# Performance work log

Hardware: AMD Instinct MI355X
Metric: run time of the kernel (lower is better)

Reference implementation:

```python
import jax, jax.numpy as jnp
import numpy as np

NUM_HEADS = 4
LN_EPS = 1e-5
ALPHA_SCALE = 2.0


def setup_inputs() -> dict:
    key = jax.random.key(0)
    ks = jax.random.split(key, 8)
    bs, C, H, W = 64, 256, 56, 56
    T, D = 6, 192
    HW = H * W
    w = lambda k, shape: (jax.random.normal(k, shape, jnp.float32) * 0.02)
    return {
        "features": jax.random.normal(ks[0], (bs, C, H, W), jnp.float32),
        "tokens": jax.random.normal(ks[1], (T, bs, D), jnp.float32),
        # mlp: Linear(HW -> T)
        "mlp_w": w(ks[2], (T, HW)), "mlp_b": jnp.zeros((T,), jnp.float32),
        # q: Linear(D -> C)
        "q_w": w(ks[3], (C, D)), "q_b": jnp.zeros((C,), jnp.float32),
        # alpha: Linear(D -> C)
        "alpha_w": w(ks[4], (C, D)), "alpha_b": jnp.zeros((C,), jnp.float32),
        # proj: Linear(C -> D)
        "proj_w": w(ks[5], (D, C)), "proj_b": jnp.zeros((D,), jnp.float32),
        "ln_g": jnp.ones((D,), jnp.float32), "ln_b": jnp.zeros((D,), jnp.float32),
    }


def reference(features, tokens, mlp_w, mlp_b, q_w, q_b,
              alpha_w, alpha_b, proj_w, proj_b, ln_g, ln_b):
    bs, C, H, W = features.shape
    T, _, D = tokens.shape
    h = NUM_HEADS
    dh = C // h
    HW = H * W
    scale = dh ** -0.5

    f = features.reshape(bs, C, HW)

    # mlp branch: Linear over HW -> [bs, C, T] -> permute to [T, bs, C]
    t_sum = jnp.einsum('bcn,tn->tbc', f, mlp_w) + mlp_b[:, None, None]

    # attn branch: few tokens attend over H*W feature map (k reused as v)
    q = jnp.einsum('tbd,cd->tbc', tokens, q_w) + q_b          # [T, bs, C]
    q = q.reshape(T, bs, h, dh).transpose(1, 2, 0, 3)         # [bs, h, T, dh]
    k = f.reshape(bs, h, dh, HW)                              # [bs, h, dh, HW]
    attn = jnp.einsum('bhtd,bhdn->bhtn', q, k) * scale        # [bs, h, T, HW]
    a = jax.nn.softmax(attn, axis=-1)
    attn_out = jnp.einsum('bhtn,bhdn->bhtd', a, k)            # [bs, h, T, dh]
    t_a = attn_out.transpose(2, 0, 1, 3).reshape(T, bs, C)
    t_sum = t_sum + t_a

    # dynamic gate: h_sigmoid(alpha(tokens)) * 2.0
    alp = jnp.clip(jnp.einsum('tbd,cd->tbc', tokens, alpha_w) + alpha_b + 3.0,
                   0.0, 6.0) / 6.0 * ALPHA_SCALE              # [T, bs, C]
    t_sum = t_sum * alp

    # proj + residual + LayerNorm (post-norm, drop_path rate 0 -> identity)
    t_sum = jnp.einsum('tbc,dc->tbd', t_sum, proj_w) + proj_b  # [T, bs, D]
    tok = tokens + t_sum
    mu = tok.mean(-1, keepdims=True)
    var = ((tok - mu) ** 2).mean(-1, keepdims=True)
    tok = (tok - mu) * jax.lax.rsqrt(var + LN_EPS) * ln_g + ln_b

    return tok, attn.reshape(bs, h, T, H, W)
```

## Files before the change

### kernel.cpp

```cpp
#include <hip/hip_runtime.h>
#include <hip/hip_bf16.h>

constexpr int BS = 64, C = 256, NH = 4, DH = 64, T = 6, D = 192;
constexpr int HW = 3136;
constexpr int NT = 112;
constexpr int S = 4, CPB = 7;
constexpr int PNF = 136;
constexpr int PNS = 116;
constexpr int QP = 72;
constexpr float SCALE = 0.125f;
constexpr float LN_EPS = 1e-5f;

typedef short bf16x8 __attribute__((ext_vector_type(8)));
typedef float f32x4 __attribute__((ext_vector_type(4)));

__device__ inline unsigned short f2bf(float x) {
    union { float f; unsigned u; } v; v.f = x;
    unsigned r = v.u + 0x7FFFu + ((v.u >> 16) & 1u);
    return (unsigned short)(r >> 16);
}

__device__ inline void st_bf8(unsigned short* dst, float4 p) {
    unsigned lo = (unsigned)f2bf(p.x) | ((unsigned)f2bf(p.y) << 16);
    unsigned hi = (unsigned)f2bf(p.z) | ((unsigned)f2bf(p.w) << 16);
    *(uint2*)dst = make_uint2(lo, hi);
}

__device__ inline int fsw(int r, int n) { return n ^ (((r >> 3) & 3) << 4); }

__device__ inline void wg_barrier_lgkm() {
    asm volatile("s_waitcnt lgkmcnt(0)" ::: "memory");
    __builtin_amdgcn_s_barrier();
    asm volatile("" ::: "memory");
}

__global__ __launch_bounds__(256) void qalpha_kernel(
    const float* __restrict__ tokens,
    const float* __restrict__ q_w,
    const float* __restrict__ q_b,
    const float* __restrict__ alpha_w,
    const float* __restrict__ alpha_b,
    float* __restrict__ q_ws,
    float* __restrict__ alp_ws)
{
    int b = blockIdx.x;
    int c = threadIdx.x;
    __shared__ float tok_s[T][D];
    for (int i = c; i < T * (D / 4); i += 256) {
        int t = i / (D / 4), v = i % (D / 4);
        *(float4*)&tok_s[t][4 * v] =
            *(const float4*)&tokens[((size_t)t * BS + b) * D + 4 * v];
    }
    __syncthreads();

    const float4* qr = (const float4*)(q_w + (size_t)c * D);
    const float4* ar = (const float4*)(alpha_w + (size_t)c * D);
    float accq[T] = {0, 0, 0, 0, 0, 0};
    float acca[T] = {0, 0, 0, 0, 0, 0};
    for (int v = 0; v < D / 4; ++v) {
        float4 qw4 = qr[v], aw4 = ar[v];
#pragma unroll
        for (int t = 0; t < T; ++t) {
            float4 t4 = *(const float4*)&tok_s[t][4 * v];
            accq[t] += qw4.x * t4.x + qw4.y * t4.y + qw4.z * t4.z + qw4.w * t4.w;
            acca[t] += aw4.x * t4.x + aw4.y * t4.y + aw4.z * t4.z + aw4.w * t4.w;
        }
    }
    float qb = q_b[c], ab = alpha_b[c];
#pragma unroll
    for (int t = 0; t < T; ++t) {
        size_t idx = ((size_t)t * BS + b) * C + c;
        q_ws[idx] = accq[t] + qb;
        float aa = acca[t] + ab + 3.0f;
        alp_ws[idx] = fminf(fmaxf(aa, 0.0f), 6.0f) * (2.0f / 6.0f);
    }
}

struct PF { float4 f0, f1, f2, f3, f4, m; };

__global__ __launch_bounds__(384) void fused_attn_mlp(
    const float* __restrict__ feat,
    const float* __restrict__ mlp_w,
    const float* __restrict__ q_ws,
    float* __restrict__ out_attn,
    float* __restrict__ o_part,
    float* __restrict__ mlp_part,
    float* __restrict__ ml_part)
{
    int bh = blockIdx.x / S, sp = blockIdx.x % S;
    int b = bh / NH, h = bh % NH;
    int tid = threadIdx.x;
    int wave = tid >> 6, lane = tid & 63;
    int col = lane & 15, quad = lane >> 4;

    __shared__ unsigned short fch[DH][PNF];
    __shared__ unsigned short pw[16][PNF];
    __shared__ unsigned short qs[16][QP];
    __shared__ float st[T][PNS];
    __shared__ float m_s[T], l_s[T], al_s[T];

    const float* fbase = feat + ((size_t)b * C + h * DH) * HW;
    float* obase = out_attn + ((size_t)bh * T) * HW;

    const int o0 = (tid / 28) * HW + 4 * (tid % 28);
    const int o1 = ((tid + 384) / 28) * HW + 4 * ((tid + 384) % 28);
    const int o2 = ((tid + 768) / 28) * HW + 4 * ((tid + 768) % 28);
    const int o3 = ((tid + 1152) / 28) * HW + 4 * ((tid + 1152) % 28);
    const int o4 = ((tid + 1536) / 28) * HW + 4 * ((tid + 1536) % 28);

    auto pf_issue = [&](PF& p, int n0) {
        p.f0 = *(const float4*)&fbase[o0 + n0];
        p.f1 = *(const float4*)&fbase[o1 + n0];
        p.f2 = *(const float4*)&fbase[o2 + n0];
        p.f3 = *(const float4*)&fbase[o3 + n0];
        if (tid < 256) p.f4 = *(const float4*)&fbase[o4 + n0];
        if (tid < 168) p.m  = *(const float4*)&mlp_w[o0 + n0];
    };
    auto pf_commit = [&](const PF& p) {
        int r0 = tid / 28,          c0 = 4 * (tid % 28);
        int r1 = (tid + 384) / 28,  c1 = 4 * ((tid + 384) % 28);
        int r2 = (tid + 768) / 28,  c2 = 4 * ((tid + 768) % 28);
        int r3 = (tid + 1152) / 28, c3 = 4 * ((tid + 1152) % 28);
        st_bf8(&fch[r0][fsw(r0, c0)], p.f0);
        st_bf8(&fch[r1][fsw(r1, c1)], p.f1);
        st_bf8(&fch[r2][fsw(r2, c2)], p.f2);
        st_bf8(&fch[r3][fsw(r3, c3)], p.f3);
        if (tid < 256) {
            int r4 = (tid + 1536) / 28, c4 = 4 * ((tid + 1536) % 28);
            st_bf8(&fch[r4][fsw(r4, c4)], p.f4);
        }
        if (tid < 168) {
            int rm = 6 + tid / 28, cm = 4 * (tid % 28);
            st_bf8(&pw[rm][fsw(rm, cm)], p.m);
        }
    };

    const int nsp = sp * CPB * NT;
    PF A;
    pf_issue(A, nsp);

    for (int i = tid; i < 16 * PNF; i += 384) pw[i / PNF][i % PNF] = 0;
    for (int i = tid; i < DH * 16; i += 384) {
        int r = i / 16;
        fch[r][fsw(r, 112 + (i % 16))] = 0;
    }
    if (tid < T) { m_s[tid] = -3e38f; l_s[tid] = 0.f; }
    qs[wave][lane] = f2bf(q_ws[((size_t)wave * BS + b) * C + h * DH + lane]);

    f32x4 accPW = {0.f, 0.f, 0.f, 0.f};
    wg_barrier_lgkm();

#pragma unroll 1
    for (int cc = 0; cc < CPB; ++cc) {
        const int n0 = nsp + cc * NT;

        pf_commit(A);
        if (cc + 1 < CPB) pf_issue(A, n0 + NT);
        wg_barrier_lgkm();

        for (int tile = wave; tile < 7; tile += 6) {
            bf16x8 a0 = *(const bf16x8*)&qs[col][quad * 8];
            bf16x8 a1 = *(const bf16x8*)&qs[col][32 + quad * 8];
            int nsw = (tile * 16 + col) ^ (quad << 4);
            bf16x8 b0, b1;
#pragma unroll
            for (int j = 0; j < 8; ++j) {
                b0[j] = (short)fch[quad * 8 + j][nsw];
                b1[j] = (short)fch[32 + quad * 8 + j][nsw];
            }
            f32x4 acc = {0.f, 0.f, 0.f, 0.f};
            acc = __builtin_amdgcn_mfma_f32_16x16x32_bf16(a0, b0, acc, 0, 0, 0);
            acc = __builtin_amdgcn_mfma_f32_16x16x32_bf16(a1, b1, acc, 0, 0, 0);
#pragma unroll
            for (int reg = 0; reg < 4; ++reg) {
                int r = quad * 4 + reg;
                if (r < 6) st[r][tile * 16 + col] = acc[reg] * SCALE;
            }
        }
        wg_barrier_lgkm();

        {
            int t = wave;
            float v0 = st[t][lane];
            float v1 = (lane + 64 < NT) ? st[t][lane + 64] : -3e38f;
            float mloc = fmaxf(v0, v1);
#pragma unroll
            for (int off = 32; off; off >>= 1) mloc = fmaxf(mloc, __shfl_down(mloc, off));
            mloc = __shfl(mloc, 0);
            float m_old = m_s[t], m_new = fmaxf(m_old, mloc);
            float p0 = __expf(v0 - m_new);
            float p1 = (lane + 64 < NT) ? __expf(v1 - m_new) : 0.f;
            pw[t][lane] = f2bf(p0);
            if (lane + 64 < NT) pw[t][lane + 64] = f2bf(p1);
            float ssum = p0 + p1;
#pragma unroll
            for (int off = 32; off; off >>= 1) ssum += __shfl_down(ssum, off);
            if (lane == 0) {
                float alpha = __expf(m_old - m_new);
                l_s[t] = l_s[t] * alpha + ssum;
                m_s[t] = m_new;
                al_s[t] = alpha;
            }
            if (lane < NT / 4) {
                *(float4*)&obase[(size_t)t * HW + n0 + 4 * lane] =
                    *(const float4*)&st[t][4 * lane];
            }
        }
        wg_barrier_lgkm();

        if (wave < 4) {
            float alpha = (col < 6) ? al_s[col] : 1.0f;
            accPW *= alpha;
            int ra = wave * 16 + col;
#pragma unroll
            for (int ks = 0; ks < 4; ++ks) {
                bf16x8 af = *(const bf16x8*)&fch[ra][fsw(ra, ks * 32 + quad * 8)];
                bf16x8 bf = *(const bf16x8*)&pw[col][fsw(col, ks * 32 + quad * 8)];
                accPW = __builtin_amdgcn_mfma_f32_16x16x32_bf16(af, bf, accPW, 0, 0, 0);
            }
        }
        wg_barrier_lgkm();
    }

    if (wave < 4) {
#pragma unroll
        for (int reg = 0; reg < 4; ++reg) {
            int c2 = wave * 16 + quad * 4 + reg;
            if (col < 6) {
                o_part[((size_t)blockIdx.x * T + col) * DH + c2] = accPW[reg];
            } else if (col < 12) {
                mlp_part[((size_t)blockIdx.x * T + (col - 6)) * DH + c2] = accPW[reg];
            }
        }
    }
    if (tid < 2 * T) {
        int t = tid >> 1;
        ml_part[((size_t)blockIdx.x * T + t) * 2 + (tid & 1)] =
            (tid & 1) ? l_s[t] : m_s[t];
    }
}

__global__ __launch_bounds__(256) void merge_proj_ln_kernel(
    const float* __restrict__ o_part,
    const float* __restrict__ mlp_part,
    const float* __restrict__ ml_part,
    const float* __restrict__ mlp_b,
    const float* __restrict__ alp_ws,
    const float* __restrict__ tokens,
    const float* __restrict__ proj_w,
    const float* __restrict__ proj_b,
    const float* __restrict__ ln_g,
    const float* __restrict__ ln_b,
    float* __restrict__ out_tok)
{
    int tb = blockIdx.x;
    int t = tb / BS, b = tb % BS;
    int tid = threadIdx.x;
    __shared__ float g_s[C];
    __shared__ float r1[4], r2[4];

    {
        int c = tid;
        int h = c >> 6, cl = c & 63;
        int bh = b * NH + h;
        float m[S], l[S];
        float M = -3e38f;
#pragma unroll
        for (int s = 0; s < S; ++s) {
            size_t blk = (size_t)(bh * S + s);
            m[s] = ml_part[(blk * T + t) * 2 + 0];
            l[s] = ml_part[(blk * T + t) * 2 + 1];
            M = fmaxf(M, m[s]);
        }
        float L = 0.f, O = 0.f, MLP = 0.f;
#pragma unroll
        for (int s = 0; s < S; ++s) {
            float w = __expf(m[s] - M);
            size_t blk = (size_t)(bh * S + s);
            size_t pidx = (blk * T + t) * DH + cl;
            L += l[s] * w;
            O += o_part[pidx] * w;
            MLP += mlp_part[pidx];
        }
        size_t idx = (size_t)tb * C + c;
        g_s[c] = (MLP + mlp_b[t] + O / L) * alp_ws[idx];
    }
    __syncthreads();

    if (tid < D) {
        int d = tid;
        float acc = proj_b[d] + tokens[(size_t)tb * D + d];
        const float4* pr = (const float4*)(proj_w + (size_t)d * C);
#pragma unroll 8
        for (int v = 0; v < C / 4; ++v) {
            float4 w4 = pr[v];
            float4 g4 = *(const float4*)&g_s[4 * v];
            acc += w4.x * g4.x + w4.y * g4.y + w4.z * g4.z + w4.w * g4.w;
        }

        float s1 = acc, s2 = acc * acc;
#pragma unroll
        for (int off = 32; off; off >>= 1) { s1 += __shfl_down(s1, off); s2 += __shfl_down(s2, off); }
        int wv = d >> 6, lane = d & 63;
        if (lane == 0) { r1[wv] = s1; r2[wv] = s2; }
        __syncthreads();
        float sum1 = r1[0] + r1[1] + r1[2];
        float sum2 = r2[0] + r2[1] + r2[2];
        float mu = sum1 * (1.0f / D);
        float var = sum2 * (1.0f / D) - mu * mu;
        float inv = rsqrtf(var + LN_EPS);
        out_tok[(size_t)tb * D + d] = (acc - mu) * inv * ln_g[d] + ln_b[d];
    } else {
        __syncthreads();
    }
}

extern "C" void kernel_launch(void* const* d_in, const int* in_sizes, int n_in,
                              void* d_out, int out_size, void* d_ws, size_t ws_size,
                              hipStream_t stream) {
    const float* features = (const float*)d_in[0];
    const float* tokens   = (const float*)d_in[1];
    const float* mlp_w    = (const float*)d_in[2];
    const float* mlp_b    = (const float*)d_in[3];
    const float* q_w      = (const float*)d_in[4];
    const float* q_b      = (const float*)d_in[5];
    const float* alpha_w  = (const float*)d_in[6];
    const float* alpha_b  = (const float*)d_in[7];
    const float* proj_w   = (const float*)d_in[8];
    const float* proj_b   = (const float*)d_in[9];
    const float* ln_g     = (const float*)d_in[10];
    const float* ln_b     = (const float*)d_in[11];

    float* out_tok  = (float*)d_out;
    float* out_attn = (float*)d_out + T * BS * D;

    constexpr int NBLK = BS * NH * S;
    float* q_ws     = (float*)d_ws;
    float* alp_ws   = q_ws + T * BS * C;
    float* ml_part  = alp_ws + T * BS * C;
    float* o_part   = ml_part + NBLK * T * 2;
    float* mlp_part = o_part + NBLK * T * DH;

    qalpha_kernel<<<BS, 256, 0, stream>>>(
        tokens, q_w, q_b, alpha_w, alpha_b, q_ws, alp_ws);

    fused_attn_mlp<<<NBLK, 384, 0, stream>>>(
        features, mlp_w, q_ws, out_attn, o_part, mlp_part, ml_part);

    merge_proj_ln_kernel<<<T * BS, 256, 0, stream>>>(
        o_part, mlp_part, ml_part, mlp_b, alp_ws, tokens,
        proj_w, proj_b, ln_g, ln_b, out_tok);
}
```

Measured before the change: 347.9 us.

## Shrink attention chunk to 64 columns, split HW 7 ways with 256-thread blocks

Reduces the per-iteration spatial chunk from 112 to 64 columns and raises the HW split from 4 to 7 blocks per (batch, head), launching 256-thread blocks instead of 384. Each wave now handles exactly one 16-column score tile and one quarter of the PV MFMA, which removes the idle waves and the zero-padded columns. The aim is more blocks, better occupancy and less LDS per block. In exchange it writes more partial results for the merge kernel and runs more barrier-separated steps per column processed.

```diff
diff --git a/kernel.cpp b/kernel.cpp
--- a/kernel.cpp
+++ b/kernel.cpp
@@ -3,10 +3,10 @@
 
 constexpr int BS = 64, C = 256, NH = 4, DH = 64, T = 6, D = 192;
 constexpr int HW = 3136;
-constexpr int NT = 112;
-constexpr int S = 4, CPB = 7;
-constexpr int PNF = 136;
-constexpr int PNS = 116;
+constexpr int NT = 64;
+constexpr int S = 7, CPB = 7;
+constexpr int PNF = 72;
+constexpr int PNS = 68;
 constexpr int QP = 72;
 constexpr float SCALE = 0.125f;
 constexpr float LN_EPS = 1e-5f;
@@ -76,9 +76,9 @@
     }
 }
 
-struct PF { float4 f0, f1, f2, f3, f4, m; };
-
-__global__ __launch_bounds__(384) void fused_attn_mlp(
+struct PF { float4 f0, f1, f2, f3, m; };
+
+__global__ __launch_bounds__(256) void fused_attn_mlp(
     const float* __restrict__ feat,
     const float* __restrict__ mlp_w,
     const float* __restrict__ q_ws,
@@ -102,35 +102,29 @@
     const float* fbase = feat + ((size_t)b * C + h * DH) * HW;
     float* obase = out_attn + ((size_t)bh * T) * HW;
 
-    const int o0 = (tid / 28) * HW + 4 * (tid % 28);
-    const int o1 = ((tid + 384) / 28) * HW + 4 * ((tid + 384) % 28);
-    const int o2 = ((tid + 768) / 28) * HW + 4 * ((tid + 768) % 28);
-    const int o3 = ((tid + 1152) / 28) * HW + 4 * ((tid + 1152) % 28);
-    const int o4 = ((tid + 1536) / 28) * HW + 4 * ((tid + 1536) % 28);
+    const int o0 = (tid / 16) * HW + 4 * (tid % 16);
+    const int o1 = ((tid + 256) / 16) * HW + 4 * ((tid + 256) % 16);
+    const int o2 = ((tid + 512) / 16) * HW + 4 * ((tid + 512) % 16);
+    const int o3 = ((tid + 768) / 16) * HW + 4 * ((tid + 768) % 16);
 
     auto pf_issue = [&](PF& p, int n0) {
         p.f0 = *(const float4*)&fbase[o0 + n0];
         p.f1 = *(const float4*)&fbase[o1 + n0];
         p.f2 = *(const float4*)&fbase[o2 + n0];
         p.f3 = *(const float4*)&fbase[o3 + n0];
-        if (tid < 256) p.f4 = *(const float4*)&fbase[o4 + n0];
-        if (tid < 168) p.m  = *(const float4*)&mlp_w[o0 + n0];
+        if (tid < 96) p.m = *(const float4*)&mlp_w[o0 + n0];
     };
     auto pf_commit = [&](const PF& p) {
-        int r0 = tid / 28,          c0 = 4 * (tid % 28);
-        int r1 = (tid + 384) / 28,  c1 = 4 * ((tid + 384) % 28);
-        int r2 = (tid + 768) / 28,  c2 = 4 * ((tid + 768) % 28);
-        int r3 = (tid + 1152) / 28, c3 = 4 * ((tid + 1152) % 28);
+        int r0 = tid / 16,         c0 = 4 * (tid % 16);
+        int r1 = (tid + 256) / 16, c1 = 4 * ((tid + 256) % 16);
+        int r2 = (tid + 512) / 16, c2 = 4 * ((tid + 512) % 16);
+        int r3 = (tid + 768) / 16, c3 = 4 * ((tid + 768) % 16);
         st_bf8(&fch[r0][fsw(r0, c0)], p.f0);
         st_bf8(&fch[r1][fsw(r1, c1)], p.f1);
         st_bf8(&fch[r2][fsw(r2, c2)], p.f2);
         st_bf8(&fch[r3][fsw(r3, c3)], p.f3);
-        if (tid < 256) {
-            int r4 = (tid + 1536) / 28, c4 = 4 * ((tid + 1536) % 28);
-            st_bf8(&fch[r4][fsw(r4, c4)], p.f4);
-        }
-        if (tid < 168) {
-            int rm = 6 + tid / 28, cm = 4 * (tid % 28);
+        if (tid < 96) {
+            int rm = 6 + tid / 16, cm = 4 * (tid % 16);
             st_bf8(&pw[rm][fsw(rm, cm)], p.m);
         }
     };
@@ -139,13 +133,12 @@
     PF A;
     pf_issue(A, nsp);
 
-    for (int i = tid; i < 16 * PNF; i += 384) pw[i / PNF][i % PNF] = 0;
-    for (int i = tid; i < DH * 16; i += 384) {
-        int r = i / 16;
-        fch[r][fsw(r, 112 + (i % 16))] = 0;
-    }
+    for (int i = tid; i < 4 * PNF; i += 256) pw[12 + i / PNF][i % PNF] = 0;
     if (tid < T) { m_s[tid] = -3e38f; l_s[tid] = 0.f; }
-    qs[wave][lane] = f2bf(q_ws[((size_t)wave * BS + b) * C + h * DH + lane]);
+    for (int i = tid; i < T * DH; i += 256) {
+        int t = i / DH, c2 = i % DH;
+        qs[t][c2] = f2bf(q_ws[((size_t)t * BS + b) * C + h * DH + c2]);
+    }
 
     f32x4 accPW = {0.f, 0.f, 0.f, 0.f};
     wg_barrier_lgkm();
@@ -158,7 +151,8 @@
         if (cc + 1 < CPB) pf_issue(A, n0 + NT);
         wg_barrier_lgkm();
 
-        for (int tile = wave; tile < 7; tile += 6) {
+        {
+            int tile = wave;
             bf16x8 a0 = *(const bf16x8*)&qs[col][quad * 8];
             bf16x8 a1 = *(const bf16x8*)&qs[col][32 + quad * 8];
             int nsw = (tile * 16 + col) ^ (quad << 4);
@@ -179,20 +173,16 @@
         }
         wg_barrier_lgkm();
 
-        {
-            int t = wave;
+        for (int t = wave; t < T; t += 4) {
             float v0 = st[t][lane];
-            float v1 = (lane + 64 < NT) ? st[t][lane + 64] : -3e38f;
-            float mloc = fmaxf(v0, v1);
+            float mloc = v0;
 #pragma unroll
             for (int off = 32; off; off >>= 1) mloc = fmaxf(mloc, __shfl_down(mloc, off));
             mloc = __shfl(mloc, 0);
             float m_old = m_s[t], m_new = fmaxf(m_old, mloc);
             float p0 = __expf(v0 - m_new);
-            float p1 = (lane + 64 < NT) ? __expf(v1 - m_new) : 0.f;
             pw[t][lane] = f2bf(p0);
-            if (lane + 64 < NT) pw[t][lane + 64] = f2bf(p1);
-            float ssum = p0 + p1;
+            float ssum = p0;
 #pragma unroll
             for (int off = 32; off; off >>= 1) ssum += __shfl_down(ssum, off);
             if (lane == 0) {
@@ -208,12 +198,12 @@
         }
         wg_barrier_lgkm();
 
-        if (wave < 4) {
+        {
             float alpha = (col < 6) ? al_s[col] : 1.0f;
             accPW *= alpha;
             int ra = wave * 16 + col;
 #pragma unroll
-            for (int ks = 0; ks < 4; ++ks) {
+            for (int ks = 0; ks < 2; ++ks) {
                 bf16x8 af = *(const bf16x8*)&fch[ra][fsw(ra, ks * 32 + quad * 8)];
                 bf16x8 bf = *(const bf16x8*)&pw[col][fsw(col, ks * 32 + quad * 8)];
                 accPW = __builtin_amdgcn_mfma_f32_16x16x32_bf16(af, bf, accPW, 0, 0, 0);
@@ -222,7 +212,7 @@
         wg_barrier_lgkm();
     }
 
-    if (wave < 4) {
+    {
 #pragma unroll
         for (int reg = 0; reg < 4; ++reg) {
             int c2 = wave * 16 + quad * 4 + reg;
@@ -344,7 +334,7 @@
     qalpha_kernel<<<BS, 256, 0, stream>>>(
         tokens, q_w, q_b, alpha_w, alpha_b, q_ws, alp_ws);
 
-    fused_attn_mlp<<<NBLK, 384, 0, stream>>>(
+    fused_attn_mlp<<<NBLK, 256, 0, stream>>>(
         features, mlp_w, q_ws, out_attn, o_part, mlp_part, ml_part);
 
     merge_proj_ln_kernel<<<T * BS, 256, 0, stream>>>(
```

New measurement: 350.5 us. Within noise of the previous version (+0.8%).
